# Kernel optimization log

Hardware: AMD Instinct MI355X
Metric: run time of the kernel (lower is better)

The kernel has to match this reference:

```python
import jax, jax.numpy as jnp
import numpy as np
from jax import lax

K = 3; PAD = 1; STR = 1; DIL = 1; DG = 16; MRM = 10.0


def _conv3(x, w, b):
    y = lax.conv_general_dilated(x, w, (1, 1), ((PAD, PAD), (PAD, PAD)),
                                 dimension_numbers=('NCHW', 'OIHW', 'NCHW'))
    return y + b[None, :, None, None]


def _leaky(x):
    return jnp.where(x >= 0, x, 0.1 * x)


def _bilinear_gather(img, py, px):
    # img: [B, dg, cg, H, W]; py, px: [B, dg, KK, H, W] sampling coords
    B, dg, cg, H, W = img.shape
    KK = py.shape[2]
    y0f = jnp.floor(py); x0f = jnp.floor(px)
    wy = py - y0f; wx = px - x0f          # bilinear fractions (grad flows via py/px)
    y0 = y0f.astype(jnp.int32); x0 = x0f.astype(jnp.int32)
    y1 = y0 + 1; x1 = x0 + 1
    imgf = img.reshape(B * dg, cg, H * W)

    def gather(yi, xi):
        valid = ((yi >= 0) & (yi < H) & (xi >= 0) & (xi < W)).astype(img.dtype)
        idx = jnp.clip(yi, 0, H - 1) * W + jnp.clip(xi, 0, W - 1)
        idxf = idx.reshape(B * dg, KK * H * W)
        v = jax.vmap(lambda im, ix: im[:, ix])(imgf, idxf)  # [B*dg, cg, KK*H*W]
        v = v.reshape(B, dg, cg, KK, H, W)
        return v * valid[:, :, None]  # zero padding outside image

    w00 = ((1 - wy) * (1 - wx))[:, :, None]
    w01 = ((1 - wy) * wx)[:, :, None]
    w10 = (wy * (1 - wx))[:, :, None]
    w11 = (wy * wx)[:, :, None]
    return (gather(y0, x0) * w00 + gather(y0, x1) * w01 +
            gather(y1, x0) * w10 + gather(y1, x1) * w11)


def reference(x, extra_feat, flow, w1, b1, w2, b2, w3, b3, weight):
    B, C, H, W = x.shape
    KK = K * K
    cg = C // DG
    P = DG * KK
    # offset/mask generating convnet
    h = _leaky(_conv3(extra_feat, w1, b1))
    h = _leaky(_conv3(h, w2, b2))
    o = _conv3(h, w3, b3)                       # [B, 3*P, H, W]
    o1, o2, m = jnp.split(o, 3, axis=1)
    off = MRM * jnp.tanh(jnp.concatenate([o1, o2], axis=1))  # [B, 2P, H, W]
    flow_yx = flow[:, ::-1]                      # flip(1): (x,y)->(y,x)
    off = off + jnp.tile(flow_yx, (1, P, 1, 1))
    off = off.reshape(B, DG, KK, 2, H, W)        # pair p=(g,k): channel 2p=y, 2p+1=x
    off_y = off[:, :, :, 0]
    off_x = off[:, :, :, 1]
    mask = jax.nn.sigmoid(m).reshape(B, DG, KK, H, W)

    ki = jnp.arange(KK)
    ky = (ki // K).astype(x.dtype) * DIL - PAD   # kernel row offsets
    kx = (ki % K).astype(x.dtype) * DIL - PAD
    base_h = jnp.arange(H, dtype=x.dtype) * STR
    base_w = jnp.arange(W, dtype=x.dtype) * STR
    py = base_h[None, None, None, :, None] + ky[None, None, :, None, None] + off_y
    px = base_w[None, None, None, None, :] + kx[None, None, :, None, None] + off_x

    img = x.reshape(B, DG, cg, H, W)
    val = _bilinear_gather(img, py, px) * mask[:, :, None]  # [B,dg,cg,KK,H,W]
    wk = weight.reshape(weight.shape[0], DG, cg, KK)
    # modulated deformable conv accumulate (bias=None in original forward)
    return jnp.einsum('bgckhw,ogck->bohw', val, wk)


def setup_inputs() -> dict:
    key = jax.random.key(0)
    ks = jax.random.split(key, 10)
    B, C, H, W = 2, 64, 128, 128
    OFFC = 3 * K * K * DG  # 432
    return {
        'x': jax.random.normal(ks[0], (B, C, H, W), jnp.float32),
        'extra_feat': jax.random.normal(ks[1], (B, 2 * C, H, W), jnp.float32),
        'flow': jax.random.normal(ks[2], (B, 2, H, W), jnp.float32),
        'w1': jax.random.normal(ks[3], (C, 2 * C, 3, 3), jnp.float32) * 0.05,
        'b1': jnp.zeros((C,), jnp.float32),
        'w2': jax.random.normal(ks[4], (C, C, 3, 3), jnp.float32) * 0.05,
        'b2': jnp.zeros((C,), jnp.float32),
        'w3': jax.random.normal(ks[5], (OFFC, C, 3, 3), jnp.float32) * 0.01,
        'b3': jnp.zeros((OFFC,), jnp.float32),
        'weight': jax.random.normal(ks[6], (C, C, 3, 3), jnp.float32) * 0.05,
    }
```

## Files before the change

kernel.cpp:

```cpp
#include <hip/hip_runtime.h>
#include <math.h>

constexpr int B_   = 2;
constexpr int C_   = 64;
constexpr int H_   = 128;
constexpr int W_   = 128;
constexpr int HW_  = H_ * W_;
constexpr int DG_  = 16;
constexpr int KK_  = 9;
constexpr int CG_  = 4;
constexpr int OFFC_ = 3 * KK_ * DG_;
constexpr int R_   = C_ * KK_;
constexpr int WP_  = 130;
constexpr int HWP_ = WP_ * WP_;

typedef _Float16 half8 __attribute__((ext_vector_type(8)));
typedef _Float16 half4 __attribute__((ext_vector_type(4)));
typedef float floatx4 __attribute__((ext_vector_type(4)));

__device__ __forceinline__ void gl_lds16(const _Float16* g, _Float16* l)
{
    __builtin_amdgcn_global_load_lds(
        (const __attribute__((address_space(1))) void*)g,
        (__attribute__((address_space(3))) void*)l, 16, 0, 0);
}

__device__ __forceinline__ int afrag_src(int c)
{
    const int cmf = c >> 6, cq = (c >> 4) & 3, cl = c & 15;
    return (cmf * 16 + cl) * 32 + cq * 8;
}

template <int OC, int CIN>
__global__ __launch_bounds__(256) void prep_wA_k(
    const float* __restrict__ w, _Float16* __restrict__ wA)
{
    constexpr int CH = CIN / 32;
    const int j = blockIdx.x * 256 + threadIdx.x;
    if (j >= 9 * CH * OC * 32) return;
    const int slab = j / (OC * 32);
    const int rem  = j - slab * (OC * 32);
    const int oc   = rem >> 5;
    const int jj   = rem & 31;
    const int t    = slab / CH;
    const int h    = slab - t * CH;
    const int ic   = h * 32 + jj;
    wA[j] = (_Float16)w[(size_t)oc * (CIN * 9) + ic * 9 + t];
}

__global__ __launch_bounds__(256) void prep_wkA_k(
    const float* __restrict__ wk, _Float16* __restrict__ wkA)
{
    const int j = blockIdx.x * 256 + threadIdx.x;
    if (j >= 18 * 64 * 32) return;
    const int s   = j >> 11;
    const int rem = j & 2047;
    const int oc  = rem >> 5;
    const int jj  = rem & 31;
    const int k   = s >> 1;
    const int gc  = (s & 1) * 32 + jj;
    wkA[j] = (_Float16)wk[(size_t)oc * R_ + gc * 9 + k];
}

template <int CC>
__global__ __launch_bounds__(256) void nchw2slabpad_f16_k(
    const float* __restrict__ in, _Float16* __restrict__ outh)
{
    const int pix = blockIdx.x * 256 + threadIdx.x;
    const int b   = blockIdx.y;
    const int yp  = pix >> 7;
    const int xp  = pix & (W_ - 1);
    const float* ib = in + (size_t)b * CC * HW_ + pix;
#pragma unroll
    for (int c0 = 0; c0 < CC; c0 += 8) {
        half8 v;
#pragma unroll
        for (int j = 0; j < 8; ++j)
            v[j] = (_Float16)ib[(size_t)(c0 + j) * HW_];
        const int slab = c0 >> 5;
        *(half8*)&outh[((size_t)(slab * B_ + b) * HWP_
                        + (size_t)(yp + 1) * WP_ + (xp + 1)) * 32 + (c0 & 31)] = v;
    }
}

__global__ __launch_bounds__(256) void nchw2gx_f16_k(
    const float* __restrict__ in, _Float16* __restrict__ outh)
{
    const int pix = blockIdx.x * 256 + threadIdx.x;
    const int b   = blockIdx.y;
    const float* ib = in + (size_t)b * C_ * HW_ + pix;
#pragma unroll
    for (int g = 0; g < DG_; ++g) {
        half4 v;
#pragma unroll
        for (int c = 0; c < 4; ++c)
            v[c] = (_Float16)ib[(size_t)(g * 4 + c) * HW_];
        *(half4*)&outh[((size_t)(b * DG_ + g) * HW_ + pix) * 4] = v;
    }
}

__global__ __launch_bounds__(256, 2) void conv1_mfma_k(
    const _Float16* __restrict__ inp, const _Float16* __restrict__ wA,
    const float* __restrict__ bias, _Float16* __restrict__ outp)
{
    __shared__ __align__(16) _Float16 Asm[2 * 4096];

    const int tid  = threadIdx.x;
    const int lane = tid & 63;
    const int wv   = tid >> 6;
    const int l15  = lane & 15;
    const int quad = lane >> 4;

    const int zx   = blockIdx.x;
    const int row  = zx >> 1;
    const int b    = row >> 7;
    const int y    = row & 127;
    const int px0  = (zx & 1) * 64 + wv * 16;

    const int sA = afrag_src(tid);

    floatx4 acc[4];
#pragma unroll
    for (int mf = 0; mf < 4; ++mf)
        acc[mf] = (floatx4){0.f, 0.f, 0.f, 0.f};

    half8 Bf[2][2];

    gl_lds16(wA + 0 * 2048 + sA, Asm + 0 * 2048 + tid * 8);
    gl_lds16(wA + 1 * 2048 + sA, Asm + 1 * 2048 + tid * 8);
#pragma unroll
    for (int j = 0; j < 2; ++j)
        Bf[0][j] = *(const half8*)&inp[
            ((size_t)(j * B_ + b) * HWP_ + (size_t)(y + 0) * WP_
             + (px0 + l15 + 0)) * 32 + quad * 8];
    __syncthreads();

#pragma unroll
    for (int p = 0; p < 18; ++p) {
        const int cur = p & 1, nxt = cur ^ 1;
        if (p < 17) {
            const int ks0 = 2 * p + 2;
            const int t = ks0 >> 2;
            const int h0 = ks0 & 3;
            const int dy = t / 3, dx = t % 3;
#pragma unroll
            for (int j = 0; j < 2; ++j) {
                gl_lds16(wA + (size_t)(ks0 + j) * 2048 + sA,
                         Asm + (nxt * 2 + j) * 2048 + tid * 8);
                Bf[nxt][j] = *(const half8*)&inp[
                    ((size_t)((h0 + j) * B_ + b) * HWP_ + (size_t)(y + dy) * WP_
                     + (px0 + l15 + dx)) * 32 + quad * 8];
            }
        }
#pragma unroll
        for (int j = 0; j < 2; ++j) {
            const _Float16* abase = Asm + (cur * 2 + j) * 2048 + lane * 8;
#pragma unroll
            for (int mf = 0; mf < 4; ++mf) {
                const half8 afr = *(const half8*)&abase[mf * 512];
                acc[mf] = __builtin_amdgcn_mfma_f32_16x16x32_f16(afr, Bf[cur][j], acc[mf], 0, 0, 0);
            }
        }
        __syncthreads();
    }

#pragma unroll
    for (int mf = 0; mf < 4; ++mf) {
        const int oc4 = mf * 16 + quad * 4;
        const float4 b4 = *(const float4*)&bias[oc4];
        half4 v4;
#pragma unroll
        for (int reg = 0; reg < 4; ++reg) {
            float r = acc[mf][reg] + ((const float*)&b4)[reg];
            r = (r >= 0.f) ? r : 0.1f * r;
            v4[reg] = (_Float16)r;
        }
        *(half4*)&outp[((size_t)((oc4 >> 5) * B_ + b) * HWP_
                        + (size_t)(y + 1) * WP_ + (px0 + l15 + 1)) * 32 + (oc4 & 31)] = v4;
    }
}

__global__ __launch_bounds__(256, 2) void conv2_mfma_k(
    const _Float16* __restrict__ inp, const _Float16* __restrict__ wA,
    const float* __restrict__ bias, _Float16* __restrict__ outp)
{
    __shared__ __align__(16) _Float16 Asm[18 * 2048];

    const int tid  = threadIdx.x;
    const int lane = tid & 63;
    const int wv   = tid >> 6;
    const int l15  = lane & 15;
    const int quad = lane >> 4;

    const int zx   = blockIdx.x;
    const int row  = zx >> 1;
    const int b    = row >> 7;
    const int y    = row & 127;
    const int px0  = (zx & 1) * 64 + wv * 16;

    const int sA = afrag_src(tid);

#pragma unroll
    for (int s = 0; s < 18; ++s)
        gl_lds16(wA + (size_t)s * 2048 + sA, Asm + s * 2048 + tid * 8);

    floatx4 acc[4];
#pragma unroll
    for (int mf = 0; mf < 4; ++mf)
        acc[mf] = (floatx4){0.f, 0.f, 0.f, 0.f};

    half8 Bf[2];
    Bf[0] = *(const half8*)&inp[
        ((size_t)(0 * B_ + b) * HWP_ + (size_t)(y + 0) * WP_
         + (px0 + l15 + 0)) * 32 + quad * 8];
    __syncthreads();

#pragma unroll
    for (int ks = 0; ks < 18; ++ks) {
        const int cur = ks & 1, nxt = cur ^ 1;
        if (ks < 17) {
            const int ks1 = ks + 1;
            const int t = ks1 >> 1, h = ks1 & 1;
            const int dy = t / 3, dx = t % 3;
            Bf[nxt] = *(const half8*)&inp[
                ((size_t)(h * B_ + b) * HWP_ + (size_t)(y + dy) * WP_
                 + (px0 + l15 + dx)) * 32 + quad * 8];
        }
        const _Float16* abase = Asm + ks * 2048 + lane * 8;
#pragma unroll
        for (int mf = 0; mf < 4; ++mf) {
            const half8 afr = *(const half8*)&abase[mf * 512];
            acc[mf] = __builtin_amdgcn_mfma_f32_16x16x32_f16(afr, Bf[cur], acc[mf], 0, 0, 0);
        }
    }

#pragma unroll
    for (int mf = 0; mf < 4; ++mf) {
        const int oc4 = mf * 16 + quad * 4;
        const float4 b4 = *(const float4*)&bias[oc4];
        half4 v4;
#pragma unroll
        for (int reg = 0; reg < 4; ++reg) {
            float r = acc[mf][reg] + ((const float*)&b4)[reg];
            r = (r >= 0.f) ? r : 0.1f * r;
            v4[reg] = (_Float16)r;
        }
        *(half4*)&outp[((size_t)((oc4 >> 5) * B_ + b) * HWP_
                        + (size_t)(y + 1) * WP_ + (px0 + l15 + 1)) * 32 + (oc4 & 31)] = v4;
    }
}

__global__ __launch_bounds__(256, 3) void conv3_mfma_k(
    const _Float16* __restrict__ h2p, const _Float16* __restrict__ w3A,
    const float* __restrict__ bias, const float* __restrict__ flow,
    _Float16* __restrict__ omh)
{
    __shared__ __align__(16) _Float16 Smem[17 * 1536];
    _Float16* Lds = Smem;

    const int tid  = threadIdx.x;
    const int lane = tid & 63;
    const int wv   = tid >> 6;
    const int l15  = lane & 15;
    const int quad = lane >> 4;

    const int row = blockIdx.x;
    const int b   = row >> 7;
    const int y   = row & 127;
    const int m0  = blockIdx.y * 48;
    const int px0 = wv * 32;

#pragma unroll
    for (int r = 0; r < 13; ++r) {
        const int c = r * 256 + tid;
        if (c < 17 * 192) {
            const int ks = c / 192;
            const int cl = c - ks * 192;
            const int cmf = cl >> 6, cq = (cl >> 4) & 3, ccl = cl & 15;
            const _Float16* src = w3A
                + ((size_t)ks * OFFC_ + m0 + cmf * 16 + ccl) * 32 + cq * 8;
            gl_lds16(src, Smem + c * 8);
        }
    }

    half8 Af17[3];
#pragma unroll
    for (int mf = 0; mf < 3; ++mf)
        Af17[mf] = *(const half8*)&w3A[
            ((size_t)17 * OFFC_ + m0 + mf * 16 + l15) * 32 + quad * 8];

    floatx4 acc[3][2];
#pragma unroll
    for (int mf = 0; mf < 3; ++mf)
#pragma unroll
        for (int nf = 0; nf < 2; ++nf)
            acc[mf][nf] = (floatx4){0.f, 0.f, 0.f, 0.f};

    half8 Bf[2][2];
#pragma unroll
    for (int nf = 0; nf < 2; ++nf)
        Bf[0][nf] = *(const half8*)&h2p[
            ((size_t)(0 * B_ + b) * HWP_ + (size_t)(y + 0) * WP_
             + (px0 + nf * 16 + l15 + 0)) * 32 + quad * 8];

    __syncthreads();

#pragma unroll
    for (int ks = 0; ks < 18; ++ks) {
        const int cur = ks & 1, nxt = cur ^ 1;
        if (ks < 17) {
            const int ks1 = ks + 1;
            const int t = ks1 >> 1, h = ks1 & 1;
            const int dy = t / 3, dx = t % 3;
#pragma unroll
            for (int nf = 0; nf < 2; ++nf)
                Bf[nxt][nf] = *(const half8*)&h2p[
                    ((size_t)(h * B_ + b) * HWP_ + (size_t)(y + dy) * WP_
                     + (px0 + nf * 16 + l15 + dx)) * 32 + quad * 8];
        }
#pragma unroll
        for (int mf = 0; mf < 3; ++mf) {
            half8 afr;
            if (ks < 17)
                afr = *(const half8*)&Smem[ks * 1536 + mf * 512 + lane * 8];
            else
                afr = Af17[mf];
            acc[mf][0] = __builtin_amdgcn_mfma_f32_16x16x32_f16(afr, Bf[cur][0], acc[mf][0], 0, 0, 0);
            acc[mf][1] = __builtin_amdgcn_mfma_f32_16x16x32_f16(afr, Bf[cur][1], acc[mf][1], 0, 0, 0);
        }
    }
    __syncthreads();

    const bool is_off = (blockIdx.y < 6);
    float flY[2], flX[2];
#pragma unroll
    for (int nf = 0; nf < 2; ++nf) {
        const int px = px0 + nf * 16 + l15;
        if (is_off) {
            flY[nf] = flow[(size_t)(b * 2 + 1) * HW_ + y * W_ + px];
            flX[nf] = flow[(size_t)(b * 2 + 0) * HW_ + y * W_ + px];
        }
    }
#pragma unroll
    for (int mf = 0; mf < 3; ++mf) {
        const float4 b4 = *(const float4*)&bias[m0 + mf * 16 + quad * 4];
#pragma unroll
        for (int nf = 0; nf < 2; ++nf) {
            const int px = px0 + nf * 16 + l15;
#pragma unroll
            for (int reg = 0; reg < 4; ++reg) {
                const int ocl = mf * 16 + quad * 4 + reg;
                float val = acc[mf][nf][reg] + ((const float*)&b4)[reg];
                if (is_off) {
                    const int slot = reg & 1;
                    const float fl = slot ? flX[nf] : flY[nf];
                    const float e = __expf(2.f * val);
                    val = 10.f * (1.f - __fdividef(2.f, e + 1.f)) + fl;
                } else {
                    val = __fdividef(1.f, 1.f + __expf(-val));
                }
                Lds[ocl * 132 + px] = (_Float16)val;
            }
        }
    }
    __syncthreads();

#pragma unroll
    for (int it = 0; it < 6; ++it) {
        const int j4 = it * 256 + tid;
        const int r  = j4 >> 5;
        const int c4 = j4 & 31;
        const int oc = m0 + r;
        int g, k, slot;
        if (oc < 2 * DG_ * KK_) {
            g = oc / 18;
            const int rem = oc - g * 18;
            k = rem >> 1;
            slot = rem & 1;
        } else {
            const int c = oc - 2 * DG_ * KK_;
            g = c / 9;
            k = c - g * 9;
            slot = 2;
        }
        const half4 hv = *(const half4*)&Lds[r * 132 + c4 * 4];
        *(half4*)&omh[((size_t)((b * DG_ * KK_ + g * KK_ + k) * 3 + slot)) * HW_
                      + y * W_ + c4 * 4] = hv;
    }
}

__global__ __launch_bounds__(256) void gather_k(
    const _Float16* __restrict__ xg, const _Float16* __restrict__ omh,
    _Float16* __restrict__ valh)
{
    const int tid = threadIdx.x;
    const int pix = blockIdx.x * 256 + tid;
    const int zy  = blockIdx.y;
    const int b   = zy / KK_;
    const int k   = zy - b * KK_;
    const int yp  = pix >> 7;
    const int xp  = pix & (W_ - 1);
    const float fy = (float)(yp + (k / 3) - 1);
    const float fx = (float)(xp + (k % 3) - 1);

    half4 rec[16];
#pragma unroll
    for (int g = 0; g < DG_; ++g) {
        const size_t obase = ((size_t)((b * DG_ + g) * KK_ + k) * 3) * HW_ + pix;
        const float oy = (float)omh[obase];
        const float ox = (float)omh[obase + HW_];
        const float m  = (float)omh[obase + 2 * HW_];

        const float py = fy + oy;
        const float px = fx + ox;
        const float y0f = floorf(py);
        const float x0f = floorf(px);
        const float wy = py - y0f;
        const float wx = px - x0f;
        const int y0 = (int)y0f, x0 = (int)x0f;
        const int y1 = y0 + 1,  x1 = x0 + 1;
        const bool vy0 = ((unsigned)y0 < (unsigned)H_);
        const bool vy1 = ((unsigned)y1 < (unsigned)H_);
        const bool vx0 = ((unsigned)x0 < (unsigned)W_);
        const bool vx1 = ((unsigned)x1 < (unsigned)W_);
        const float w00 = vy0 && vx0 ? (1.f - wy) * (1.f - wx) : 0.f;
        const float w01 = vy0 && vx1 ? (1.f - wy) * wx         : 0.f;
        const float w10 = vy1 && vx0 ? wy * (1.f - wx)         : 0.f;
        const float w11 = vy1 && vx1 ? wy * wx                 : 0.f;
        const int i00 = (vy0 && vx0) ? y0 * W_ + x0 : 0;
        const int i01 = (vy0 && vx1) ? y0 * W_ + x1 : 0;
        const int i10 = (vy1 && vx0) ? y1 * W_ + x0 : 0;
        const int i11 = (vy1 && vx1) ? y1 * W_ + x1 : 0;

        const _Float16* xb = xg + (size_t)(b * DG_ + g) * HW_ * 4;
        const half4 p00 = *(const half4*)&xb[(size_t)i00 * 4];
        const half4 p01 = *(const half4*)&xb[(size_t)i01 * 4];
        const half4 p10 = *(const half4*)&xb[(size_t)i10 * 4];
        const half4 p11 = *(const half4*)&xb[(size_t)i11 * 4];

        half4 v4;
#pragma unroll
        for (int c = 0; c < CG_; ++c) {
            float v = w00 * (float)p00[c] + w01 * (float)p01[c]
                    + w10 * (float)p10[c] + w11 * (float)p11[c];
            v4[c] = (_Float16)(v * m);
        }
        rec[g] = v4;
    }

    _Float16* r0 = &valh[((size_t)((2 * k) * B_ + b) * HW_ + pix) * 32];
    _Float16* r1 = &valh[((size_t)((2 * k + 1) * B_ + b) * HW_ + pix) * 32];
#pragma unroll
    for (int j = 0; j < 4; ++j) {
        half8 w0, w1;
#pragma unroll
        for (int c = 0; c < 4; ++c) {
            w0[c]     = rec[2 * j][c];
            w0[c + 4] = rec[2 * j + 1][c];
            w1[c]     = rec[8 + 2 * j][c];
            w1[c + 4] = rec[9 + 2 * j][c];
        }
        *(half8*)&r0[j * 8] = w0;
        *(half8*)&r1[j * 8] = w1;
    }
}

__global__ __launch_bounds__(256, 2) void einsum_mfma_k(
    const _Float16* __restrict__ valh, const _Float16* __restrict__ wkA,
    float* __restrict__ out)
{
    __shared__ __align__(16) _Float16 Smem[18 * 2048];
    float* Lds = (float*)Smem;

    const int tid  = threadIdx.x;
    const int lane = tid & 63;
    const int wv   = tid >> 6;
    const int l15  = lane & 15;
    const int quad = lane >> 4;

    const int pixg0 = blockIdx.x * 64 + wv * 16;
    const int b     = pixg0 >> 14;
    const int pix0  = pixg0 & (HW_ - 1);

    const int sA = afrag_src(tid);

#pragma unroll
    for (int s = 0; s < 18; ++s)
        gl_lds16(wkA + (size_t)s * 2048 + sA, Smem + s * 2048 + tid * 8);

    floatx4 acc[4];
#pragma unroll
    for (int mf = 0; mf < 4; ++mf)
        acc[mf] = (floatx4){0.f, 0.f, 0.f, 0.f};

    half8 Bf[2];
    Bf[0] = *(const half8*)&valh[((size_t)(0 * B_ + b) * HW_ + pix0 + l15) * 32 + quad * 8];
    __syncthreads();

#pragma unroll
    for (int s = 0; s < 18; ++s) {
        const int cur = s & 1, nxt = cur ^ 1;
        if (s < 17) {
            const int s1 = s + 1;
            Bf[nxt] = *(const half8*)&valh[
                ((size_t)(s1 * B_ + b) * HW_ + pix0 + l15) * 32 + quad * 8];
        }
        const _Float16* abase = Smem + s * 2048 + lane * 8;
#pragma unroll
        for (int mf = 0; mf < 4; ++mf) {
            const half8 afr = *(const half8*)&abase[mf * 512];
            acc[mf] = __builtin_amdgcn_mfma_f32_16x16x32_f16(afr, Bf[cur], acc[mf], 0, 0, 0);
        }
    }
    __syncthreads();

    const int pxl = wv * 16 + l15;
#pragma unroll
    for (int mf = 0; mf < 4; ++mf)
#pragma unroll
        for (int reg = 0; reg < 4; ++reg)
            Lds[(mf * 16 + quad * 4 + reg) * 68 + pxl] = acc[mf][reg];
    __syncthreads();

    const int pixb = blockIdx.x * 64 & (HW_ - 1);
#pragma unroll
    for (int it = 0; it < 4; ++it) {
        const int j4 = it * 256 + tid;
        const int r  = j4 >> 4;
        const int c4 = j4 & 15;
        float4 v;
        v.x = Lds[r * 68 + c4 * 4 + 0];
        v.y = Lds[r * 68 + c4 * 4 + 1];
        v.z = Lds[r * 68 + c4 * 4 + 2];
        v.w = Lds[r * 68 + c4 * 4 + 3];
        *(float4*)&out[((size_t)(b * C_ + r)) * HW_ + pixb + c4 * 4] = v;
    }
}

extern "C" void kernel_launch(void* const* d_in, const int* in_sizes, int n_in,
                              void* d_out, int out_size, void* d_ws, size_t ws_size,
                              hipStream_t stream)
{
    const float* x    = (const float*)d_in[0];
    const float* ef   = (const float*)d_in[1];
    const float* flow = (const float*)d_in[2];
    const float* w1   = (const float*)d_in[3];
    const float* b1   = (const float*)d_in[4];
    const float* w2   = (const float*)d_in[5];
    const float* b2   = (const float*)d_in[6];
    const float* w3   = (const float*)d_in[7];
    const float* b3   = (const float*)d_in[8];
    const float* wk   = (const float*)d_in[9];
    float* out = (float*)d_out;

    _Float16* omh  = (_Float16*)d_ws;
    _Float16* valh = omh + (size_t)B_ * OFFC_ * HW_;
    _Float16* ef_p = valh + (size_t)18 * B_ * HW_ * 32;
    _Float16* xg   = ef_p + (size_t)4 * B_ * HWP_ * 32;
    _Float16* h1p  = xg + (size_t)B_ * HW_ * 64;
    _Float16* h2p  = h1p + (size_t)2 * B_ * HWP_ * 32;
    _Float16* w1A  = h2p + (size_t)2 * B_ * HWP_ * 32;
    _Float16* w2A  = w1A + 64 * 128 * 9;
    _Float16* w3A  = w2A + 64 * 64 * 9;
    _Float16* wkA  = w3A + OFFC_ * 64 * 9;

    hipMemsetAsync(ef_p, 0, (size_t)4 * B_ * HWP_ * 32 * 2, stream);
    hipMemsetAsync(h1p, 0, (size_t)2 * B_ * HWP_ * 32 * 2, stream);
    hipMemsetAsync(h2p, 0, (size_t)2 * B_ * HWP_ * 32 * 2, stream);

    prep_wA_k<64, 128><<<dim3((64 * 128 * 9 + 255) / 256), 256, 0, stream>>>(w1, w1A);
    prep_wA_k<64, 64><<<dim3((64 * 64 * 9 + 255) / 256), 256, 0, stream>>>(w2, w2A);
    prep_wA_k<OFFC_, 64><<<dim3((OFFC_ * 64 * 9 + 255) / 256), 256, 0, stream>>>(w3, w3A);
    prep_wkA_k<<<dim3((18 * 64 * 32 + 255) / 256), 256, 0, stream>>>(wk, wkA);
    nchw2slabpad_f16_k<128><<<dim3(HW_ / 256, B_), 256, 0, stream>>>(ef, ef_p);
    nchw2gx_f16_k<<<dim3(HW_ / 256, B_), 256, 0, stream>>>(x, xg);

    conv1_mfma_k<<<dim3(B_ * H_ * 2), 256, 0, stream>>>(ef_p, w1A, b1, h1p);
    conv2_mfma_k<<<dim3(B_ * H_ * 2), 256, 0, stream>>>(h1p, w2A, b2, h2p);
    conv3_mfma_k<<<dim3(B_ * H_, 9), 256, 0, stream>>>(h2p, w3A, b3, flow, omh);

    gather_k<<<dim3(HW_ / 256, B_ * KK_), 256, 0, stream>>>(xg, omh, valh);
    einsum_mfma_k<<<dim3(B_ * HW_ / 64), 256, 0, stream>>>(valh, wkA, out);
}
```

Before: 208.2 us.

## Stage conv3 input rows in LDS and split each row across two blocks

The conv3 kernel now splits each output row into two 64-pixel halves, doubling the grid. The needed input slab (3 rows × 68 columns × both channel halves) is copied into LDS once with async global-to-LDS loads, so the nine taps reuse it instead of each wave fetching from global memory per step. The last six weight slices are held in registers and the first twelve in LDS. This raises LDS usage to about 63 KB and lowers the occupancy hint to 2 blocks per CU, trading more blocks and reuse against fewer resident waves and less MFMA work per wave.

```diff
diff --git a/kernel.cpp b/kernel.cpp
--- a/kernel.cpp
+++ b/kernel.cpp
@@ -250,12 +250,14 @@
     }
 }
 
-__global__ __launch_bounds__(256, 3) void conv3_mfma_k(
+__global__ __launch_bounds__(256, 2) void conv3_mfma_k(
     const _Float16* __restrict__ h2p, const _Float16* __restrict__ w3A,
     const float* __restrict__ bias, const float* __restrict__ flow,
     _Float16* __restrict__ omh)
 {
-    __shared__ __align__(16) _Float16 Smem[17 * 1536];
+    __shared__ __align__(16) _Float16 Smem[31488];
+    _Float16* Asm = Smem;
+    _Float16* Bsm = Smem + 18432;
     _Float16* Lds = Smem;
 
     const int tid  = threadIdx.x;
@@ -264,112 +266,104 @@
     const int l15  = lane & 15;
     const int quad = lane >> 4;
 
-    const int row = blockIdx.x;
-    const int b   = row >> 7;
-    const int y   = row & 127;
-    const int m0  = blockIdx.y * 48;
-    const int px0 = wv * 32;
-
-#pragma unroll
-    for (int r = 0; r < 13; ++r) {
-        const int c = r * 256 + tid;
-        if (c < 17 * 192) {
-            const int ks = c / 192;
-            const int cl = c - ks * 192;
-            const int cmf = cl >> 6, cq = (cl >> 4) & 3, ccl = cl & 15;
-            const _Float16* src = w3A
-                + ((size_t)ks * OFFC_ + m0 + cmf * 16 + ccl) * 32 + cq * 8;
-            gl_lds16(src, Smem + c * 8);
-        }
-    }
-
-    half8 Af17[3];
+    const int zx   = blockIdx.x;
+    const int row  = zx >> 1;
+    const int b    = row >> 7;
+    const int y    = row & 127;
+    const int px0b = (zx & 1) * 64;
+    const int pxw  = wv * 16;
+    const int m0   = blockIdx.y * 48;
+
+#pragma unroll
+    for (int r = 0; r < 9; ++r) {
+        const int c  = r * 256 + tid;
+        const int ks = c / 192;
+        const int cl = c - ks * 192;
+        const int cmf = cl >> 6, cq = (cl >> 4) & 3, ccl = cl & 15;
+        gl_lds16(w3A + ((size_t)ks * OFFC_ + m0 + cmf * 16 + ccl) * 32 + cq * 8,
+                 Asm + c * 8);
+    }
+#pragma unroll
+    for (int r = 0; r < 7; ++r) {
+        const int cb = r * 256 + tid;
+        if (cb < 1632) {
+            const int plane = cb / 68;
+            const int pxl   = cb - plane * 68;
+            const int h  = plane / 12;
+            const int rm = plane - h * 12;
+            const int dy = rm >> 2;
+            const int q  = rm & 3;
+            int col = px0b + pxl; if (col > 129) col = 129;
+            gl_lds16(h2p + ((size_t)(h * B_ + b) * HWP_
+                            + (size_t)(y + dy) * WP_ + col) * 32 + q * 8,
+                     Bsm + cb * 8);
+        }
+    }
+    half8 Areg[6][3];
+#pragma unroll
+    for (int s = 0; s < 6; ++s)
+#pragma unroll
+        for (int mf = 0; mf < 3; ++mf)
+            Areg[s][mf] = *(const half8*)&w3A[
+                ((size_t)(12 + s) * OFFC_ + m0 + mf * 16 + l15) * 32 + quad * 8];
+
+    floatx4 acc[3];
 #pragma unroll
     for (int mf = 0; mf < 3; ++mf)
-        Af17[mf] = *(const half8*)&w3A[
-            ((size_t)17 * OFFC_ + m0 + mf * 16 + l15) * 32 + quad * 8];
-
-    floatx4 acc[3][2];
-#pragma unroll
-    for (int mf = 0; mf < 3; ++mf)
-#pragma unroll
-        for (int nf = 0; nf < 2; ++nf)
-            acc[mf][nf] = (floatx4){0.f, 0.f, 0.f, 0.f};
-
-    half8 Bf[2][2];
-#pragma unroll
-    for (int nf = 0; nf < 2; ++nf)
-        Bf[0][nf] = *(const half8*)&h2p[
-            ((size_t)(0 * B_ + b) * HWP_ + (size_t)(y + 0) * WP_
-             + (px0 + nf * 16 + l15 + 0)) * 32 + quad * 8];
+        acc[mf] = (floatx4){0.f, 0.f, 0.f, 0.f};
 
     __syncthreads();
 
 #pragma unroll
     for (int ks = 0; ks < 18; ++ks) {
-        const int cur = ks & 1, nxt = cur ^ 1;
-        if (ks < 17) {
-            const int ks1 = ks + 1;
-            const int t = ks1 >> 1, h = ks1 & 1;
-            const int dy = t / 3, dx = t % 3;
-#pragma unroll
-            for (int nf = 0; nf < 2; ++nf)
-                Bf[nxt][nf] = *(const half8*)&h2p[
-                    ((size_t)(h * B_ + b) * HWP_ + (size_t)(y + dy) * WP_
-                     + (px0 + nf * 16 + l15 + dx)) * 32 + quad * 8];
-        }
+        const int t = ks >> 1, h = ks & 1;
+        const int dy = t / 3, dx = t % 3;
+        const half8 bfr = *(const half8*)&Bsm[
+            ((((h * 3 + dy) << 2) + quad) * 68 + pxw + l15 + dx) * 8];
 #pragma unroll
         for (int mf = 0; mf < 3; ++mf) {
             half8 afr;
-            if (ks < 17)
-                afr = *(const half8*)&Smem[ks * 1536 + mf * 512 + lane * 8];
+            if (ks < 12)
+                afr = *(const half8*)&Asm[ks * 1536 + mf * 512 + lane * 8];
             else
-                afr = Af17[mf];
-            acc[mf][0] = __builtin_amdgcn_mfma_f32_16x16x32_f16(afr, Bf[cur][0], acc[mf][0], 0, 0, 0);
-            acc[mf][1] = __builtin_amdgcn_mfma_f32_16x16x32_f16(afr, Bf[cur][1], acc[mf][1], 0, 0, 0);
+                afr = Areg[ks - 12][mf];
+            acc[mf] = __builtin_amdgcn_mfma_f32_16x16x32_f16(afr, bfr, acc[mf], 0, 0, 0);
         }
     }
     __syncthreads();
 
     const bool is_off = (blockIdx.y < 6);
-    float flY[2], flX[2];
-#pragma unroll
-    for (int nf = 0; nf < 2; ++nf) {
-        const int px = px0 + nf * 16 + l15;
-        if (is_off) {
-            flY[nf] = flow[(size_t)(b * 2 + 1) * HW_ + y * W_ + px];
-            flX[nf] = flow[(size_t)(b * 2 + 0) * HW_ + y * W_ + px];
-        }
+    const int px = px0b + pxw + l15;
+    float flY = 0.f, flX = 0.f;
+    if (is_off) {
+        flY = flow[(size_t)(b * 2 + 1) * HW_ + y * W_ + px];
+        flX = flow[(size_t)(b * 2 + 0) * HW_ + y * W_ + px];
     }
 #pragma unroll
     for (int mf = 0; mf < 3; ++mf) {
         const float4 b4 = *(const float4*)&bias[m0 + mf * 16 + quad * 4];
 #pragma unroll
-        for (int nf = 0; nf < 2; ++nf) {
-            const int px = px0 + nf * 16 + l15;
-#pragma unroll
-            for (int reg = 0; reg < 4; ++reg) {
-                const int ocl = mf * 16 + quad * 4 + reg;
-                float val = acc[mf][nf][reg] + ((const float*)&b4)[reg];
-                if (is_off) {
-                    const int slot = reg & 1;
-                    const float fl = slot ? flX[nf] : flY[nf];
-                    const float e = __expf(2.f * val);
-                    val = 10.f * (1.f - __fdividef(2.f, e + 1.f)) + fl;
-                } else {
-                    val = __fdividef(1.f, 1.f + __expf(-val));
-                }
-                Lds[ocl * 132 + px] = (_Float16)val;
+        for (int reg = 0; reg < 4; ++reg) {
+            const int ocl = mf * 16 + quad * 4 + reg;
+            float val = acc[mf][reg] + ((const float*)&b4)[reg];
+            if (is_off) {
+                const int slot = reg & 1;
+                const float fl = slot ? flX : flY;
+                const float e = __expf(2.f * val);
+                val = 10.f * (1.f - __fdividef(2.f, e + 1.f)) + fl;
+            } else {
+                val = __fdividef(1.f, 1.f + __expf(-val));
             }
-        }
-    }
-    __syncthreads();
-
-#pragma unroll
-    for (int it = 0; it < 6; ++it) {
+            Lds[ocl * 68 + pxw + l15] = (_Float16)val;
+        }
+    }
+    __syncthreads();
+
+#pragma unroll
+    for (int it = 0; it < 3; ++it) {
         const int j4 = it * 256 + tid;
-        const int r  = j4 >> 5;
-        const int c4 = j4 & 31;
+        const int r  = j4 >> 4;
+        const int c4 = j4 & 15;
         const int oc = m0 + r;
         int g, k, slot;
         if (oc < 2 * DG_ * KK_) {
@@ -383,9 +377,9 @@
             k = c - g * 9;
             slot = 2;
         }
-        const half4 hv = *(const half4*)&Lds[r * 132 + c4 * 4];
+        const half4 hv = *(const half4*)&Lds[r * 68 + c4 * 4];
         *(half4*)&omh[((size_t)((b * DG_ * KK_ + g * KK_ + k) * 3 + slot)) * HW_
-                      + y * W_ + c4 * 4] = hv;
+                      + y * W_ + px0b + c4 * 4] = hv;
     }
 }
 
@@ -577,7 +571,7 @@
 
     conv1_mfma_k<<<dim3(B_ * H_ * 2), 256, 0, stream>>>(ef_p, w1A, b1, h1p);
     conv2_mfma_k<<<dim3(B_ * H_ * 2), 256, 0, stream>>>(h1p, w2A, b2, h2p);
-    conv3_mfma_k<<<dim3(B_ * H_, 9), 256, 0, stream>>>(h2p, w3A, b3, flow, omh);
+    conv3_mfma_k<<<dim3(B_ * H_ * 2, 9), 256, 0, stream>>>(h2p, w3A, b3, flow, omh);
 
     gather_k<<<dim3(HW_ / 256, B_ * KK_), 256, 0, stream>>>(xg, omh, valh);
     einsum_mfma_k<<<dim3(B_ * HW_ / 64), 256, 0, stream>>>(valh, wkA, out);
```

Measured after the change: 223.3 us. 1.07x slower.
